# Performance work log

Measured on AMD Instinct MI355X. Metric: run time of the kernel, lower is better.

The kernel has to match this reference:

```python
import jax, jax.numpy as jnp
import numpy as np

FOCUS_RADIUS = 20.0
FOCUS_WEIGHT = 10.0
SPREAD_PENALTY = 1.0
EPS = 1e-8


def setup_inputs() -> dict:
    key = jax.random.key(0)
    k1, k2 = jax.random.split(key)
    B, WL, H, W = 16, 8, 512, 512
    predictions = jax.random.uniform(k1, (B, WL, H, W), dtype=jnp.float32)
    targets = jax.random.uniform(k2, (B, WL, H, W), dtype=jnp.float32)
    return {"predictions": predictions, "targets": targets}


def reference(predictions, targets):
    B, WL, H, W = predictions.shape
    dt = predictions.dtype
    ys = jnp.arange(H, dtype=dt)[:, None]   # [H,1]
    xs = jnp.arange(W, dtype=dt)[None, :]   # [1,W]

    # base MSE loss
    base_loss = jnp.mean((predictions - targets) ** 2)

    # target energy centroids (detached in the original via .item())
    tsum = targets.sum((-2, -1))                      # [B,WL]
    valid = tsum >= EPS                               # center exists
    ts_safe = jnp.where(valid, tsum, 1.0)
    cy = jax.lax.stop_gradient((targets * ys).sum((-2, -1)) / ts_safe)  # [B,WL]
    cx = jax.lax.stop_gradient((targets * xs).sum((-2, -1)) / ts_safe)  # [B,WL]

    # squared distance to target center, per image  [B,WL,H,W]
    dist_sq = (ys - cy[..., None, None]) ** 2 + (xs - cx[..., None, None]) ** 2
    focus_mask = (dist_sq <= FOCUS_RADIUS * FOCUS_RADIUS).astype(dt)

    pred_total = predictions.sum((-2, -1))            # [B,WL]
    focus_energy = (predictions * focus_mask).sum((-2, -1))
    spread = (predictions * dist_sq).sum((-2, -1))
    pt_safe = jnp.where(pred_total > EPS, pred_total, 1.0)

    active = valid & (pred_total > EPS)
    focus_loss = jnp.sum(jnp.where(active, (1.0 - focus_energy / pt_safe) ** 2, 0.0))
    spread_loss = jnp.sum(jnp.where(active, spread / pt_safe, 0.0))

    return base_loss + FOCUS_WEIGHT * focus_loss + SPREAD_PENALTY * spread_loss
```

## Files before the change

### kernel.cpp

```cpp
#include <hip/hip_runtime.h>


#define HH 512
#define WW 512
#define IMG_PIX (HH * WW)
#define VEC_PER_IMG (IMG_PIX / 4)
#define BLOCKS_PER_IMG 16
#define VEC_PER_BLK (VEC_PER_IMG / BLOCKS_PER_IMG)
#define THREADS 256
#define ITERS (VEC_PER_BLK / THREADS)
#define EPSF 1e-8f
#define R2 400.0f

__device__ __forceinline__ float wave_reduce_sum(float v) {
    v += __shfl_down(v, 32);
    v += __shfl_down(v, 16);
    v += __shfl_down(v, 8);
    v += __shfl_down(v, 4);
    v += __shfl_down(v, 2);
    v += __shfl_down(v, 1);
    return v;
}

__device__ __forceinline__ double wave_reduce_sum_d(double v) {
    v += __shfl_down(v, 32);
    v += __shfl_down(v, 16);
    v += __shfl_down(v, 8);
    v += __shfl_down(v, 4);
    v += __shfl_down(v, 2);
    v += __shfl_down(v, 1);
    return v;
}

__global__ void __launch_bounds__(THREADS) stream_kernel(
        const float4* __restrict__ pred, const float4* __restrict__ tgt,
        float* __restrict__ acc) {
    const int img = blockIdx.x / BLOCKS_PER_IMG;
    const int sub = blockIdx.x % BLOCKS_PER_IMG;
    const int base = img * VEC_PER_IMG + sub * VEC_PER_BLK;

    float ts = 0.f, ty = 0.f, tx = 0.f, mse = 0.f;
    float m0 = 0.f, my = 0.f, mx = 0.f, m2 = 0.f;

#pragma unroll 4
    for (int j = 0; j < ITERS; ++j) {
        const int i = j * THREADS + threadIdx.x;
        const int vidx = base + i;
        const float4 tv = tgt[vidx];
        const float4 pv = pred[vidx];
        const int pix = (sub * VEC_PER_BLK + i) << 2;
        const float y  = (float)(pix >> 9);
        const float x0 = (float)(pix & 511);
        const float x1 = x0 + 1.f, x2 = x0 + 2.f, x3 = x0 + 3.f;

        const float tsum = tv.x + tv.y + tv.z + tv.w;
        ts += tsum;
        ty += y * tsum;
        tx += x0 * tv.x + x1 * tv.y + x2 * tv.z + x3 * tv.w;

        const float d0 = pv.x - tv.x, d1 = pv.y - tv.y,
                    d2 = pv.z - tv.z, d3 = pv.w - tv.w;
        mse += d0 * d0 + d1 * d1 + d2 * d2 + d3 * d3;

        const float psum = pv.x + pv.y + pv.z + pv.w;
        m0 += psum;
        my += y * psum;
        mx += x0 * pv.x + x1 * pv.y + x2 * pv.z + x3 * pv.w;
        const float y2 = y * y;
        m2 += pv.x * (y2 + x0 * x0) + pv.y * (y2 + x1 * x1)
            + pv.z * (y2 + x2 * x2) + pv.w * (y2 + x3 * x3);
    }

    float vals[8] = {ts, ty, tx, mse, m0, my, mx, m2};
    __shared__ float red[4][8];
    const int wid = threadIdx.x >> 6, lane = threadIdx.x & 63;
#pragma unroll
    for (int k = 0; k < 8; ++k) vals[k] = wave_reduce_sum(vals[k]);
    if (lane == 0)
#pragma unroll
        for (int k = 0; k < 8; ++k) red[wid][k] = vals[k];
    __syncthreads();
    if (threadIdx.x < 8) {
        const int k = threadIdx.x;
        const float s = red[0][k] + red[1][k] + red[2][k] + red[3][k];
        atomicAdd(&acc[img * 8 + k], s);
    }
}

__global__ void __launch_bounds__(64) focus_kernel(
        const float* __restrict__ pred, const float* __restrict__ acc,
        float* __restrict__ fe_out) {
    const int img = blockIdx.x;
    const float ts = acc[img * 8 + 0];
    float fe = 0.f;
    if (ts >= EPSF) {
        const float cy = acc[img * 8 + 1] / ts;
        const float cx = acc[img * 8 + 2] / ts;
        const int ylo = max(0, (int)ceilf(cy - 20.f) - 1);
        const int yhi = min(HH - 1, (int)floorf(cy + 20.f) + 1);
        const int xlo = max(0, (int)ceilf(cx - 20.f) - 1);
        const int xhi = min(WW - 1, (int)floorf(cx + 20.f) + 1);
        const float* p = pred + (size_t)img * IMG_PIX;
        const int xx = xlo + (int)threadIdx.x;
        if (xx <= xhi) {
            const float dx = (float)xx - cx;
            const float dx2 = dx * dx;
            for (int y = ylo; y <= yhi; ++y) {
                const float dy = (float)y - cy;
                if (dy * dy + dx2 <= R2) fe += p[(y << 9) + xx];
            }
        }
    }
    fe = wave_reduce_sum(fe);
    if (threadIdx.x == 0) fe_out[img] = fe;
}

__global__ void __launch_bounds__(128) final_kernel(
        const float* __restrict__ acc, const float* __restrict__ fe,
        float* __restrict__ out, int nimg, float inv_n) {
    const int i = threadIdx.x;
    double v = 0.0, m = 0.0;
    if (i < nimg) {
        const float* a = acc + i * 8;
        m = (double)a[3];
        const float ts = a[0];
        const float pt = a[4];
        if (ts >= EPSF && pt > EPSF) {
            const double cy = (double)a[1] / (double)ts;
            const double cx = (double)a[2] / (double)ts;
            const double spread = (double)a[7] - 2.0 * cy * (double)a[5]
                                - 2.0 * cx * (double)a[6]
                                + (cy * cy + cx * cx) * (double)a[4];
            const double r = 1.0 - (double)fe[i] / (double)pt;
            v = 10.0 * r * r + spread / (double)pt;
        }
    }
    __shared__ double redv[2], redm[2];
    v = wave_reduce_sum_d(v);
    m = wave_reduce_sum_d(m);
    if ((i & 63) == 0) { redv[i >> 6] = v; redm[i >> 6] = m; }
    __syncthreads();
    if (i == 0)
        out[0] = (float)((redm[0] + redm[1]) * (double)inv_n + redv[0] + redv[1]);
}

extern "C" void kernel_launch(void* const* d_in, const int* in_sizes, int n_in,
                              void* d_out, int out_size, void* d_ws, size_t ws_size,
                              hipStream_t stream) {
    const float* pred = (const float*)d_in[0];
    const float* tgt  = (const float*)d_in[1];
    float* out = (float*)d_out;
    float* ws  = (float*)d_ws;

    const int n = in_sizes[0];
    const int nimg = n / IMG_PIX;

    float* acc = ws;
    float* fe  = ws + nimg * 8;

    hipMemsetAsync(ws, 0, (size_t)nimg * 9 * sizeof(float), stream);

    const int grid = nimg * BLOCKS_PER_IMG;
    stream_kernel<<<grid, THREADS, 0, stream>>>(
        (const float4*)pred, (const float4*)tgt, acc);
    focus_kernel<<<nimg, 64, 0, stream>>>(pred, acc, fe);
    final_kernel<<<1, 128, 0, stream>>>(acc, fe, out, nimg, 1.0f / (float)n);
}
```

Measured before the change: 63.86 us.

## Replace atomics and memset with per-block partials, add nontemporal target loads

Each stream block now writes its eight partial sums to its own slot in a workspace array instead of atomically adding into per-image accumulators, so the hipMemsetAsync can be dropped. The focus and final kernels reduce the 16 partials per image themselves. Target loads use a nontemporal hint so they do not displace prediction data the focus kernel rereads, and the unroll factor goes from 4 to 8. The change saves a memset launch and atomic traffic, in exchange for slightly more work in the small downstream kernels.

After: 63.92 us. No clear change (+0.1%).

```diff
diff --git a/kernel.cpp b/kernel.cpp
--- a/kernel.cpp
+++ b/kernel.cpp
@@ -11,6 +11,8 @@
 #define ITERS (VEC_PER_BLK / THREADS)
 #define EPSF 1e-8f
 #define R2 400.0f
+
+typedef float f4 __attribute__((ext_vector_type(4)));
 
 __device__ __forceinline__ float wave_reduce_sum(float v) {
     v += __shfl_down(v, 32);
@@ -33,8 +35,8 @@
 }
 
 __global__ void __launch_bounds__(THREADS) stream_kernel(
-        const float4* __restrict__ pred, const float4* __restrict__ tgt,
-        float* __restrict__ acc) {
+        const f4* __restrict__ pred, const f4* __restrict__ tgt,
+        float* __restrict__ part) {
     const int img = blockIdx.x / BLOCKS_PER_IMG;
     const int sub = blockIdx.x % BLOCKS_PER_IMG;
     const int base = img * VEC_PER_IMG + sub * VEC_PER_BLK;
@@ -42,33 +44,33 @@
     float ts = 0.f, ty = 0.f, tx = 0.f, mse = 0.f;
     float m0 = 0.f, my = 0.f, mx = 0.f, m2 = 0.f;
 
-#pragma unroll 4
+#pragma unroll 8
     for (int j = 0; j < ITERS; ++j) {
         const int i = j * THREADS + threadIdx.x;
         const int vidx = base + i;
-        const float4 tv = tgt[vidx];
-        const float4 pv = pred[vidx];
+        const f4 tv = __builtin_nontemporal_load(&tgt[vidx]);
+        const f4 pv = pred[vidx];
         const int pix = (sub * VEC_PER_BLK + i) << 2;
         const float y  = (float)(pix >> 9);
         const float x0 = (float)(pix & 511);
         const float x1 = x0 + 1.f, x2 = x0 + 2.f, x3 = x0 + 3.f;
 
-        const float tsum = tv.x + tv.y + tv.z + tv.w;
+        const float tsum = tv[0] + tv[1] + tv[2] + tv[3];
         ts += tsum;
         ty += y * tsum;
-        tx += x0 * tv.x + x1 * tv.y + x2 * tv.z + x3 * tv.w;
+        tx += x0 * tv[0] + x1 * tv[1] + x2 * tv[2] + x3 * tv[3];
 
-        const float d0 = pv.x - tv.x, d1 = pv.y - tv.y,
-                    d2 = pv.z - tv.z, d3 = pv.w - tv.w;
+        const float d0 = pv[0] - tv[0], d1 = pv[1] - tv[1],
+                    d2 = pv[2] - tv[2], d3 = pv[3] - tv[3];
         mse += d0 * d0 + d1 * d1 + d2 * d2 + d3 * d3;
 
-        const float psum = pv.x + pv.y + pv.z + pv.w;
+        const float psum = pv[0] + pv[1] + pv[2] + pv[3];
         m0 += psum;
         my += y * psum;
-        mx += x0 * pv.x + x1 * pv.y + x2 * pv.z + x3 * pv.w;
+        mx += x0 * pv[0] + x1 * pv[1] + x2 * pv[2] + x3 * pv[3];
         const float y2 = y * y;
-        m2 += pv.x * (y2 + x0 * x0) + pv.y * (y2 + x1 * x1)
-            + pv.z * (y2 + x2 * x2) + pv.w * (y2 + x3 * x3);
+        m2 += pv[0] * (y2 + x0 * x0) + pv[1] * (y2 + x1 * x1)
+            + pv[2] * (y2 + x2 * x2) + pv[3] * (y2 + x3 * x3);
     }
 
     float vals[8] = {ts, ty, tx, mse, m0, my, mx, m2};
@@ -82,26 +84,34 @@
     __syncthreads();
     if (threadIdx.x < 8) {
         const int k = threadIdx.x;
-        const float s = red[0][k] + red[1][k] + red[2][k] + red[3][k];
-        atomicAdd(&acc[img * 8 + k], s);
+        part[blockIdx.x * 8 + k] = red[0][k] + red[1][k] + red[2][k] + red[3][k];
     }
 }
 
 __global__ void __launch_bounds__(64) focus_kernel(
-        const float* __restrict__ pred, const float* __restrict__ acc,
+        const float* __restrict__ pred, const float* __restrict__ part,
         float* __restrict__ fe_out) {
     const int img = blockIdx.x;
-    const float ts = acc[img * 8 + 0];
+    const int lane = threadIdx.x;
+    float ts = 0.f, ty = 0.f, tx = 0.f;
+    if (lane < BLOCKS_PER_IMG) {
+        const float* p = part + (img * BLOCKS_PER_IMG + lane) * 8;
+        ts = p[0]; ty = p[1]; tx = p[2];
+    }
+    ts = __shfl(wave_reduce_sum(ts), 0);
+    ty = __shfl(wave_reduce_sum(ty), 0);
+    tx = __shfl(wave_reduce_sum(tx), 0);
+
     float fe = 0.f;
     if (ts >= EPSF) {
-        const float cy = acc[img * 8 + 1] / ts;
-        const float cx = acc[img * 8 + 2] / ts;
+        const float cy = ty / ts;
+        const float cx = tx / ts;
         const int ylo = max(0, (int)ceilf(cy - 20.f) - 1);
         const int yhi = min(HH - 1, (int)floorf(cy + 20.f) + 1);
         const int xlo = max(0, (int)ceilf(cx - 20.f) - 1);
         const int xhi = min(WW - 1, (int)floorf(cx + 20.f) + 1);
         const float* p = pred + (size_t)img * IMG_PIX;
-        const int xx = xlo + (int)threadIdx.x;
+        const int xx = xlo + lane;
         if (xx <= xhi) {
             const float dx = (float)xx - cx;
             const float dx2 = dx * dx;
@@ -112,27 +122,38 @@
         }
     }
     fe = wave_reduce_sum(fe);
-    if (threadIdx.x == 0) fe_out[img] = fe;
+    if (lane == 0) fe_out[img] = fe;
 }
 
 __global__ void __launch_bounds__(128) final_kernel(
-        const float* __restrict__ acc, const float* __restrict__ fe,
+        const float* __restrict__ part, const float* __restrict__ fe,
         float* __restrict__ out, int nimg, float inv_n) {
     const int i = threadIdx.x;
     double v = 0.0, m = 0.0;
     if (i < nimg) {
-        const float* a = acc + i * 8;
-        m = (double)a[3];
-        const float ts = a[0];
-        const float pt = a[4];
-        if (ts >= EPSF && pt > EPSF) {
-            const double cy = (double)a[1] / (double)ts;
-            const double cx = (double)a[2] / (double)ts;
-            const double spread = (double)a[7] - 2.0 * cy * (double)a[5]
-                                - 2.0 * cx * (double)a[6]
-                                + (cy * cy + cx * cx) * (double)a[4];
-            const double r = 1.0 - (double)fe[i] / (double)pt;
-            v = 10.0 * r * r + spread / (double)pt;
+        float ts = 0.f, mse = 0.f, m0 = 0.f, myv = 0.f, mxv = 0.f, m2 = 0.f;
+        float tyv = 0.f, txv = 0.f;
+        const float* p = part + i * BLOCKS_PER_IMG * 8;
+#pragma unroll
+        for (int s = 0; s < BLOCKS_PER_IMG; ++s) {
+            ts  += p[s * 8 + 0];
+            tyv += p[s * 8 + 1];
+            txv += p[s * 8 + 2];
+            mse += p[s * 8 + 3];
+            m0  += p[s * 8 + 4];
+            myv += p[s * 8 + 5];
+            mxv += p[s * 8 + 6];
+            m2  += p[s * 8 + 7];
+        }
+        m = (double)mse;
+        if (ts >= EPSF && m0 > EPSF) {
+            const double cy = (double)tyv / (double)ts;
+            const double cx = (double)txv / (double)ts;
+            const double spread = (double)m2 - 2.0 * cy * (double)myv
+                                - 2.0 * cx * (double)mxv
+                                + (cy * cy + cx * cx) * (double)m0;
+            const double r = 1.0 - (double)fe[i] / (double)m0;
+            v = 10.0 * r * r + spread / (double)m0;
         }
     }
     __shared__ double redv[2], redm[2];
@@ -154,15 +175,13 @@
 
     const int n = in_sizes[0];
     const int nimg = n / IMG_PIX;
+    const int nblk = nimg * BLOCKS_PER_IMG;
 
-    float* acc = ws;
-    float* fe  = ws + nimg * 8;
+    float* part = ws;
+    float* fe   = ws + nblk * 8;
 
-    hipMemsetAsync(ws, 0, (size_t)nimg * 9 * sizeof(float), stream);
-
-    const int grid = nimg * BLOCKS_PER_IMG;
-    stream_kernel<<<grid, THREADS, 0, stream>>>(
-        (const float4*)pred, (const float4*)tgt, acc);
-    focus_kernel<<<nimg, 64, 0, stream>>>(pred, acc, fe);
-    final_kernel<<<1, 128, 0, stream>>>(acc, fe, out, nimg, 1.0f / (float)n);
+    stream_kernel<<<nblk, THREADS, 0, stream>>>(
+        (const f4*)pred, (const f4*)tgt, part);
+    focus_kernel<<<nimg, 64, 0, stream>>>(pred, part, fe);
+    final_kernel<<<1, 128, 0, stream>>>(part, fe, out, nimg, 1.0f / (float)n);
 }
```
